# Optimization experiments

Measured on AMD Instinct MI355X. Metric: run time of the kernel, lower is better.

The kernel has to match this reference:

```python
import jax, jax.numpy as jnp
import numpy as np

B = 16384
MOTION = 128      # motion_size
USED = 3          # used_motions
LAT = 32          # latent_size
H1 = 512
H2 = 512
MOE = 8
IN = MOTION * (USED - 1) + LAT  # 288 (used_angles = 0)


def setup_inputs() -> dict:
    key = jax.random.key(0)
    ks = jax.random.split(key, 14)
    s = 0.02
    return {
        "motions": jax.random.normal(ks[0], (B, MOTION * (USED - 1)), jnp.float32),
        "z": jax.random.normal(ks[1], (B, LAT), jnp.float32),
        # gate MLP params
        "gw1": jax.random.normal(ks[2], (IN, H1), jnp.float32) * s,
        "gb1": jnp.zeros((H1,), jnp.float32),
        "gw2": jax.random.normal(ks[3], (H1, H2), jnp.float32) * s,
        "gb2": jnp.zeros((H2,), jnp.float32),
        "gw3": jax.random.normal(ks[4], (H2, MOE), jnp.float32) * s,
        "gb3": jnp.zeros((MOE,), jnp.float32),
        # stacked expert params: layer k weight [MOE, in_k, out_k]
        "W1": jax.random.normal(ks[5], (MOE, IN, H1), jnp.float32) * s,
        "b1": jnp.zeros((MOE, H1), jnp.float32),
        "W2": jax.random.normal(ks[6], (MOE, H1 + LAT, H2), jnp.float32) * s,
        "b2": jnp.zeros((MOE, H2), jnp.float32),
        "W3": jax.random.normal(ks[7], (MOE, H2 + LAT, MOTION), jnp.float32) * s,
        "b3": jnp.zeros((MOE, MOTION), jnp.float32),
    }


def reference(motions, z, gw1, gb1, gw2, gb2, gw3, gb3, W1, b1, W2, b2, W3, b3):
    # used_angles == 0 -> angles is empty; input = concat([motions, z])
    x = jnp.concatenate([motions, z], axis=1)            # [B, IN]

    # gate: 3-layer ELU MLP -> per-expert blend weights [B, MOE]
    para = jax.nn.elu(x @ gw1 + gb1)
    para = jax.nn.elu(para @ gw2 + gb2)
    para = jax.nn.elu(para @ gw3 + gb3)

    # all experts batched via stacked weights (replaces Python loop)
    zb = jnp.broadcast_to(z[None], (MOE, B, LAT))        # z re-concatenated per layer
    h = jax.nn.elu(jnp.einsum('bi,eio->ebo', x, W1) + b1[:, None, :])              # [E,B,H1]
    h = jax.nn.elu(jnp.einsum('ebi,eio->ebo', jnp.concatenate([h, zb], -1), W2)
                   + b2[:, None, :])                                               # [E,B,H2]
    h = jax.nn.elu(jnp.einsum('ebi,eio->ebo', jnp.concatenate([h, zb], -1), W3)
                   + b3[:, None, :])                                               # [E,B,M]

    # gated combine, then divide by Frobenius norm of the whole gate matrix
    out = jnp.einsum('be,ebm->bm', para, h)              # [B, MOTION]
    out = out / jnp.linalg.norm(para)
    return jax.nn.sigmoid(out)
```

## Files before the change

### kernel.cpp

```cpp
#include <hip/hip_runtime.h>


typedef __attribute__((ext_vector_type(8))) short bf16x8;
typedef __attribute__((ext_vector_type(4))) float f32x4;
#define MFMA(a, b, c) __builtin_amdgcn_mfma_f32_16x16x32_bf16(a, b, c, 0, 0, 0)

#define STRIDE 552
#define XSTRIDE 296

__device__ __forceinline__ float elu_f(float x) { return x > 0.f ? x : (__expf(x) - 1.f); }

__device__ __forceinline__ ushort f2bf(float f) {
    union { float f; unsigned u; } v; v.f = f;
    unsigned r = v.u + 0x7fffu + ((v.u >> 16) & 1u);
    return (ushort)(r >> 16);
}
__device__ __forceinline__ float bf2f(ushort u) {
    union { unsigned u; float f; } v; v.u = ((unsigned)u) << 16;
    return v.f;
}
__device__ __forceinline__ bf16x8 ldg8(const ushort* p) { return *(const bf16x8*)p; }

__global__ void prep_xz(const float* __restrict__ motions, const float* __restrict__ z,
                        ushort* __restrict__ xz) {
    int i = blockIdx.x * 256 + threadIdx.x;
    int r = i / 72, c = i % 72;
    float4 v = (c < 64) ? ((const float4*)motions)[r * 64 + c]
                        : ((const float4*)z)[r * 8 + (c - 64)];
    ushort4 o;
    o.x = f2bf(v.x); o.y = f2bf(v.y); o.z = f2bf(v.z); o.w = f2bf(v.w);
    *(ushort4*)(xz + (size_t)r * 288 + c * 4) = o;
}

__global__ void prep_transpose(const float* __restrict__ in, ushort* __restrict__ out,
                               int K, int N) {
    __shared__ float tile[32][33];
    const int e = blockIdx.z;
    const float* inp = in + (size_t)e * K * N;
    ushort* outp = out + (size_t)e * N * K;
    const int k0 = blockIdx.x * 32, n0 = blockIdx.y * 32;
    const int tx = threadIdx.x, ty = threadIdx.y;
    #pragma unroll
    for (int i = 0; i < 4; ++i)
        tile[ty + i * 8][tx] = inp[(size_t)(k0 + ty + i * 8) * N + n0 + tx];
    __syncthreads();
    #pragma unroll
    for (int i = 0; i < 4; ++i)
        outp[(size_t)(n0 + ty + i * 8) * K + k0 + tx] = f2bf(tile[tx][ty + i * 8]);
}

__global__ __launch_bounds__(1024, 1) void gate_kernel(
    const ushort* __restrict__ xz,
    const ushort* __restrict__ gw1t, const float* __restrict__ gb1,
    const ushort* __restrict__ gw2t, const float* __restrict__ gb2,
    const float* __restrict__ gw3, const float* __restrict__ gb3,
    float* __restrict__ para, float* __restrict__ partial)
{
    __shared__ ushort hs[64 * STRIDE];
    __shared__ float red[512];
    const int t = threadIdx.x;
    const int lane = t & 63, w = t >> 6;
    const int lr = lane & 15, lk = lane >> 4;
    const int r0 = blockIdx.x * 64;
    const ushort* xrow = xz + (size_t)r0 * 288;
    const int n0 = w * 32;

    {
        const ushort* B0 = gw1t + (size_t)(n0 + lr) * 288 + lk * 8;
        const ushort* B1 = gw1t + (size_t)(n0 + 16 + lr) * 288 + lk * 8;
        f32x4 acc[4][2] = {};
        bf16x8 bc0 = ldg8(B0), bc1 = ldg8(B1);
        for (int ks = 0; ks < 9; ++ks) {
            bf16x8 bn0 = bc0, bn1 = bc1;
            if (ks < 8) { bn0 = ldg8(B0 + (ks + 1) * 32); bn1 = ldg8(B1 + (ks + 1) * 32); }
            bf16x8 a[4];
            #pragma unroll
            for (int mf = 0; mf < 4; ++mf)
                a[mf] = ldg8(xrow + (size_t)(mf * 16 + lr) * 288 + ks * 32 + lk * 8);
            #pragma unroll
            for (int mf = 0; mf < 4; ++mf) {
                acc[mf][0] = MFMA(a[mf], bc0, acc[mf][0]);
                acc[mf][1] = MFMA(a[mf], bc1, acc[mf][1]);
            }
            bc0 = bn0; bc1 = bn1;
        }
        #pragma unroll
        for (int nf = 0; nf < 2; ++nf) {
            int col = n0 + nf * 16 + lr;
            float bb = gb1[col];
            #pragma unroll
            for (int mf = 0; mf < 4; ++mf)
                #pragma unroll
                for (int j = 0; j < 4; ++j)
                    hs[(mf * 16 + lk * 4 + j) * STRIDE + col] = f2bf(elu_f(acc[mf][nf][j] + bb));
        }
    }
    __syncthreads();

    {
        const ushort* B0 = gw2t + (size_t)(n0 + lr) * 512 + lk * 8;
        const ushort* B1 = gw2t + (size_t)(n0 + 16 + lr) * 512 + lk * 8;
        f32x4 acc[4][2] = {};
        bf16x8 bc0 = ldg8(B0), bc1 = ldg8(B1);
        for (int ks = 0; ks < 16; ++ks) {
            bf16x8 bn0 = bc0, bn1 = bc1;
            if (ks < 15) { bn0 = ldg8(B0 + (ks + 1) * 32); bn1 = ldg8(B1 + (ks + 1) * 32); }
            bf16x8 a[4];
            #pragma unroll
            for (int mf = 0; mf < 4; ++mf)
                a[mf] = *(const bf16x8*)&hs[(mf * 16 + lr) * STRIDE + ks * 32 + lk * 8];
            #pragma unroll
            for (int mf = 0; mf < 4; ++mf) {
                acc[mf][0] = MFMA(a[mf], bc0, acc[mf][0]);
                acc[mf][1] = MFMA(a[mf], bc1, acc[mf][1]);
            }
            bc0 = bn0; bc1 = bn1;
        }
        __syncthreads();
        #pragma unroll
        for (int nf = 0; nf < 2; ++nf) {
            int col = n0 + nf * 16 + lr;
            float bb = gb2[col];
            #pragma unroll
            for (int mf = 0; mf < 4; ++mf)
                #pragma unroll
                for (int j = 0; j < 4; ++j)
                    hs[(mf * 16 + lk * 4 + j) * STRIDE + col] = f2bf(elu_f(acc[mf][nf][j] + bb));
        }
    }
    __syncthreads();

    if (t < 512) {
        const int row = t >> 3, e = t & 7;
        float acc = 0.f;
        for (int k = 0; k < 512; k += 8) {
            uint4 hv = *(const uint4*)&hs[row * STRIDE + k];
            acc += bf2f((ushort)(hv.x)) * gw3[(k + 0) * 8 + e];
            acc += bf2f((ushort)(hv.x >> 16)) * gw3[(k + 1) * 8 + e];
            acc += bf2f((ushort)(hv.y)) * gw3[(k + 2) * 8 + e];
            acc += bf2f((ushort)(hv.y >> 16)) * gw3[(k + 3) * 8 + e];
            acc += bf2f((ushort)(hv.z)) * gw3[(k + 4) * 8 + e];
            acc += bf2f((ushort)(hv.z >> 16)) * gw3[(k + 5) * 8 + e];
            acc += bf2f((ushort)(hv.w)) * gw3[(k + 6) * 8 + e];
            acc += bf2f((ushort)(hv.w >> 16)) * gw3[(k + 7) * 8 + e];
        }
        float p = elu_f(acc + gb3[e]);
        para[(size_t)(r0 + row) * 8 + e] = p;
        red[t] = p * p;
    }
    __syncthreads();
    for (int s = 256; s >= 1; s >>= 1) {
        if (t < s) red[t] += red[t + s];
        __syncthreads();
    }
    if (t == 0) partial[blockIdx.x] = red[0];
}

__global__ void finalize_kernel(const float* __restrict__ partial, float* __restrict__ invn) {
    __shared__ float red[256];
    const int t = threadIdx.x;
    red[t] = partial[t];
    __syncthreads();
    for (int s = 128; s >= 1; s >>= 1) {
        if (t < s) red[t] += red[t + s];
        __syncthreads();
    }
    if (t == 0) invn[0] = 1.0f / sqrtf(red[0]);
}

__global__ __launch_bounds__(1024, 1) void expert_kernel(
    const ushort* __restrict__ xz, const float* __restrict__ z,
    const ushort* __restrict__ W1t, const float* __restrict__ b1,
    const ushort* __restrict__ W2t, const float* __restrict__ b2,
    const ushort* __restrict__ W3t, const float* __restrict__ b3,
    const float* __restrict__ para, const float* __restrict__ invn,
    float* __restrict__ out)
{
    __shared__ ushort hs[64 * STRIDE];
    __shared__ ushort xs[64 * XSTRIDE];
    __shared__ float ps[64 * 8];
    const int t = threadIdx.x;
    const int lane = t & 63, w = t >> 6;
    const int lr = lane & 15, lk = lane >> 4;
    const int r0 = blockIdx.x * 64;
    const int n0 = w * 32;
    const int rb = (w >> 2) * 16;
    const int c0 = (w & 3) * 32;

    for (int i = t; i < 2304; i += 1024) {
        int r = i / 36, c = i % 36;
        *(uint4*)&xs[r * XSTRIDE + c * 8] = *(const uint4*)(xz + (size_t)(r0 + r) * 288 + c * 8);
    }
    for (int i = t; i < 2048; i += 1024) {
        int r = i >> 5, c = i & 31;
        hs[r * STRIDE + 512 + c] = f2bf(z[(size_t)(r0 + r) * 32 + c]);
    }
    if (t < 512) ps[t] = para[(size_t)r0 * 8 + t];
    const float inv_norm = invn[0];

    f32x4 oacc[2] = {};

    for (int e = 0; e < 8; ++e) {
        __syncthreads();

        {
            const ushort* Wt = W1t + (size_t)e * 512 * 288;
            const ushort* B0 = Wt + (size_t)(n0 + lr) * 288 + lk * 8;
            const ushort* B1 = Wt + (size_t)(n0 + 16 + lr) * 288 + lk * 8;
            f32x4 acc[4][2] = {};
            bf16x8 bc0 = ldg8(B0), bc1 = ldg8(B1);
            for (int ks = 0; ks < 9; ++ks) {
                bf16x8 bn0 = bc0, bn1 = bc1;
                if (ks < 8) { bn0 = ldg8(B0 + (ks + 1) * 32); bn1 = ldg8(B1 + (ks + 1) * 32); }
                bf16x8 a[4];
                #pragma unroll
                for (int mf = 0; mf < 4; ++mf)
                    a[mf] = *(const bf16x8*)&xs[(mf * 16 + lr) * XSTRIDE + ks * 32 + lk * 8];
                #pragma unroll
                for (int mf = 0; mf < 4; ++mf) {
                    acc[mf][0] = MFMA(a[mf], bc0, acc[mf][0]);
                    acc[mf][1] = MFMA(a[mf], bc1, acc[mf][1]);
                }
                bc0 = bn0; bc1 = bn1;
            }
            #pragma unroll
            for (int nf = 0; nf < 2; ++nf) {
                int col = n0 + nf * 16 + lr;
                float bb = b1[e * 512 + col];
                #pragma unroll
                for (int mf = 0; mf < 4; ++mf)
                    #pragma unroll
                    for (int j = 0; j < 4; ++j)
                        hs[(mf * 16 + lk * 4 + j) * STRIDE + col] = f2bf(elu_f(acc[mf][nf][j] + bb));
            }
        }
        __syncthreads();

        {
            const ushort* Wt = W2t + (size_t)e * 512 * 544;
            const ushort* B0 = Wt + (size_t)(n0 + lr) * 544 + lk * 8;
            const ushort* B1 = Wt + (size_t)(n0 + 16 + lr) * 544 + lk * 8;
            f32x4 acc[4][2] = {};
            bf16x8 bc0 = ldg8(B0), bc1 = ldg8(B1);
            for (int ks = 0; ks < 17; ++ks) {
                bf16x8 bn0 = bc0, bn1 = bc1;
                if (ks < 16) { bn0 = ldg8(B0 + (ks + 1) * 32); bn1 = ldg8(B1 + (ks + 1) * 32); }
                bf16x8 a[4];
                #pragma unroll
                for (int mf = 0; mf < 4; ++mf)
                    a[mf] = *(const bf16x8*)&hs[(mf * 16 + lr) * STRIDE + ks * 32 + lk * 8];
                #pragma unroll
                for (int mf = 0; mf < 4; ++mf) {
                    acc[mf][0] = MFMA(a[mf], bc0, acc[mf][0]);
                    acc[mf][1] = MFMA(a[mf], bc1, acc[mf][1]);
                }
                bc0 = bn0; bc1 = bn1;
            }
            __syncthreads();
            #pragma unroll
            for (int nf = 0; nf < 2; ++nf) {
                int col = n0 + nf * 16 + lr;
                float bb = b2[e * 512 + col];
                #pragma unroll
                for (int mf = 0; mf < 4; ++mf)
                    #pragma unroll
                    for (int j = 0; j < 4; ++j)
                        hs[(mf * 16 + lk * 4 + j) * STRIDE + col] = f2bf(elu_f(acc[mf][nf][j] + bb));
            }
        }
        __syncthreads();

        {
            const ushort* Wt = W3t + (size_t)e * 128 * 544;
            const ushort* B0 = Wt + (size_t)(c0 + lr) * 544 + lk * 8;
            const ushort* B1 = Wt + (size_t)(c0 + 16 + lr) * 544 + lk * 8;
            f32x4 acc3[2] = {};
            bf16x8 bc0 = ldg8(B0), bc1 = ldg8(B1);
            for (int ks = 0; ks < 17; ++ks) {
                bf16x8 bn0 = bc0, bn1 = bc1;
                if (ks < 16) { bn0 = ldg8(B0 + (ks + 1) * 32); bn1 = ldg8(B1 + (ks + 1) * 32); }
                bf16x8 a = *(const bf16x8*)&hs[(rb + lr) * STRIDE + ks * 32 + lk * 8];
                acc3[0] = MFMA(a, bc0, acc3[0]);
                acc3[1] = MFMA(a, bc1, acc3[1]);
                bc0 = bn0; bc1 = bn1;
            }
            #pragma unroll
            for (int nf = 0; nf < 2; ++nf) {
                float bb = b3[e * 128 + c0 + nf * 16 + lr];
                #pragma unroll
                for (int j = 0; j < 4; ++j) {
                    int row = rb + lk * 4 + j;
                    float h3 = elu_f(acc3[nf][j] + bb);
                    oacc[nf][j] += ps[row * 8 + e] * h3;
                }
            }
        }
    }

    #pragma unroll
    for (int nf = 0; nf < 2; ++nf)
        #pragma unroll
        for (int j = 0; j < 4; ++j) {
            int row = rb + lk * 4 + j;
            float v = oacc[nf][j] * inv_norm;
            out[(size_t)(r0 + row) * 128 + c0 + nf * 16 + lr] = 1.0f / (1.0f + __expf(-v));
        }
}

extern "C" void kernel_launch(void* const* d_in, const int* in_sizes, int n_in,
                              void* d_out, int out_size, void* d_ws, size_t ws_size,
                              hipStream_t stream) {
    const float* motions = (const float*)d_in[0];
    const float* z   = (const float*)d_in[1];
    const float* gw1 = (const float*)d_in[2];
    const float* gb1 = (const float*)d_in[3];
    const float* gw2 = (const float*)d_in[4];
    const float* gb2 = (const float*)d_in[5];
    const float* gw3 = (const float*)d_in[6];
    const float* gb3 = (const float*)d_in[7];
    const float* W1  = (const float*)d_in[8];
    const float* b1  = (const float*)d_in[9];
    const float* W2  = (const float*)d_in[10];
    const float* b2  = (const float*)d_in[11];
    const float* W3  = (const float*)d_in[12];
    const float* b3  = (const float*)d_in[13];
    float* out = (float*)d_out;

    char* W = (char*)d_ws;
    ushort* xz      = (ushort*)(W);
    ushort* gw1t    = (ushort*)(W + 9437184);
    ushort* gw2t    = (ushort*)(W + 9732096);
    ushort* W1t     = (ushort*)(W + 10256384);
    ushort* W2t     = (ushort*)(W + 12615680);
    ushort* W3t     = (ushort*)(W + 17072128);
    float*  para    = (float*) (W + 18186240);
    float*  partial = (float*) (W + 18710528);
    float*  invn    = (float*) (W + 18711552);

    prep_xz<<<dim3(4608), dim3(256), 0, stream>>>(motions, z, xz);
    prep_transpose<<<dim3(9, 16, 1), dim3(32, 8), 0, stream>>>(gw1, gw1t, 288, 512);
    prep_transpose<<<dim3(16, 16, 1), dim3(32, 8), 0, stream>>>(gw2, gw2t, 512, 512);
    prep_transpose<<<dim3(9, 16, 8), dim3(32, 8), 0, stream>>>(W1, W1t, 288, 512);
    prep_transpose<<<dim3(17, 16, 8), dim3(32, 8), 0, stream>>>(W2, W2t, 544, 512);
    prep_transpose<<<dim3(17, 4, 8), dim3(32, 8), 0, stream>>>(W3, W3t, 544, 128);

    gate_kernel<<<dim3(256), dim3(1024), 0, stream>>>(xz, gw1t, gb1, gw2t, gb2, gw3, gb3,
                                                      para, partial);
    finalize_kernel<<<dim3(1), dim3(256), 0, stream>>>(partial, invn);
    expert_kernel<<<dim3(256), dim3(1024), 0, stream>>>(xz, z, W1t, b1, W2t, b2, W3t, b3,
                                                        para, invn, out);
}
```

Baseline: 283.7 us.

## Split experts across two block halves and combine partials in a separate kernel

The expert kernel now launches 512 blocks, with each half handling four experts for a 64-row tile, and writes unnormalized partial sums to two buffers. A new combine kernel adds the partials, applies the inverse norm and the sigmoid. The shared-memory staging of the input tile is removed in favour of direct global loads, and launch bounds ask for two blocks per CU so occupancy can rise on a 256-CU part. The cost is an extra output-sized round trip through memory, an extra launch, and heavier register pressure under the tighter bounds.

```diff
diff --git a/kernel.cpp b/kernel.cpp
--- a/kernel.cpp
+++ b/kernel.cpp
@@ -6,7 +6,6 @@
 #define MFMA(a, b, c) __builtin_amdgcn_mfma_f32_16x16x32_bf16(a, b, c, 0, 0, 0)
 
 #define STRIDE 552
-#define XSTRIDE 296
 
 __device__ __forceinline__ float elu_f(float x) { return x > 0.f ? x : (__expf(x) - 1.f); }
 
@@ -168,39 +167,37 @@
     if (t == 0) invn[0] = 1.0f / sqrtf(red[0]);
 }
 
-__global__ __launch_bounds__(1024, 1) void expert_kernel(
+__global__ __launch_bounds__(1024, 2) void expert_kernel(
     const ushort* __restrict__ xz, const float* __restrict__ z,
     const ushort* __restrict__ W1t, const float* __restrict__ b1,
     const ushort* __restrict__ W2t, const float* __restrict__ b2,
     const ushort* __restrict__ W3t, const float* __restrict__ b3,
-    const float* __restrict__ para, const float* __restrict__ invn,
-    float* __restrict__ out)
+    const float* __restrict__ para,
+    float* __restrict__ part0, float* __restrict__ part1)
 {
     __shared__ ushort hs[64 * STRIDE];
-    __shared__ ushort xs[64 * XSTRIDE];
     __shared__ float ps[64 * 8];
     const int t = threadIdx.x;
     const int lane = t & 63, w = t >> 6;
     const int lr = lane & 15, lk = lane >> 4;
-    const int r0 = blockIdx.x * 64;
+    const int tile = blockIdx.x & 255;
+    const int half = blockIdx.x >> 8;
+    const int r0 = tile * 64;
+    const ushort* xrow = xz + (size_t)r0 * 288;
     const int n0 = w * 32;
     const int rb = (w >> 2) * 16;
     const int c0 = (w & 3) * 32;
 
-    for (int i = t; i < 2304; i += 1024) {
-        int r = i / 36, c = i % 36;
-        *(uint4*)&xs[r * XSTRIDE + c * 8] = *(const uint4*)(xz + (size_t)(r0 + r) * 288 + c * 8);
-    }
     for (int i = t; i < 2048; i += 1024) {
         int r = i >> 5, c = i & 31;
         hs[r * STRIDE + 512 + c] = f2bf(z[(size_t)(r0 + r) * 32 + c]);
     }
     if (t < 512) ps[t] = para[(size_t)r0 * 8 + t];
-    const float inv_norm = invn[0];
 
     f32x4 oacc[2] = {};
-
-    for (int e = 0; e < 8; ++e) {
+    const int e0 = half * 4;
+
+    for (int e = e0; e < e0 + 4; ++e) {
         __syncthreads();
 
         {
@@ -215,7 +212,7 @@
                 bf16x8 a[4];
                 #pragma unroll
                 for (int mf = 0; mf < 4; ++mf)
-                    a[mf] = *(const bf16x8*)&xs[(mf * 16 + lr) * XSTRIDE + ks * 32 + lk * 8];
+                    a[mf] = ldg8(xrow + (size_t)(mf * 16 + lr) * 288 + ks * 32 + lk * 8);
                 #pragma unroll
                 for (int mf = 0; mf < 4; ++mf) {
                     acc[mf][0] = MFMA(a[mf], bc0, acc[mf][0]);
@@ -297,14 +294,27 @@
         }
     }
 
+    float* dst = half ? part1 : part0;
     #pragma unroll
     for (int nf = 0; nf < 2; ++nf)
         #pragma unroll
         for (int j = 0; j < 4; ++j) {
             int row = rb + lk * 4 + j;
-            float v = oacc[nf][j] * inv_norm;
-            out[(size_t)(r0 + row) * 128 + c0 + nf * 16 + lr] = 1.0f / (1.0f + __expf(-v));
-        }
+            dst[(size_t)(r0 + row) * 128 + c0 + nf * 16 + lr] = oacc[nf][j];
+        }
+}
+
+__global__ void combine_kernel(float* __restrict__ out, const float* __restrict__ part1,
+                               const float* __restrict__ invn) {
+    const int i = blockIdx.x * 256 + threadIdx.x;
+    const float inv = invn[0];
+    float4 a = ((const float4*)out)[i];
+    float4 b = ((const float4*)part1)[i];
+    a.x = 1.0f / (1.0f + __expf(-(a.x + b.x) * inv));
+    a.y = 1.0f / (1.0f + __expf(-(a.y + b.y) * inv));
+    a.z = 1.0f / (1.0f + __expf(-(a.z + b.z) * inv));
+    a.w = 1.0f / (1.0f + __expf(-(a.w + b.w) * inv));
+    ((float4*)out)[i] = a;
 }
 
 extern "C" void kernel_launch(void* const* d_in, const int* in_sizes, int n_in,
@@ -336,6 +346,7 @@
     float*  para    = (float*) (W + 18186240);
     float*  partial = (float*) (W + 18710528);
     float*  invn    = (float*) (W + 18711552);
+    float*  part1   = (float*) (W + 18720768);
 
     prep_xz<<<dim3(4608), dim3(256), 0, stream>>>(motions, z, xz);
     prep_transpose<<<dim3(9, 16, 1), dim3(32, 8), 0, stream>>>(gw1, gw1t, 288, 512);
@@ -347,6 +358,7 @@
     gate_kernel<<<dim3(256), dim3(1024), 0, stream>>>(xz, gw1t, gb1, gw2t, gb2, gw3, gb3,
                                                       para, partial);
     finalize_kernel<<<dim3(1), dim3(256), 0, stream>>>(partial, invn);
-    expert_kernel<<<dim3(256), dim3(1024), 0, stream>>>(xz, z, W1t, b1, W2t, b2, W3t, b3,
-                                                        para, invn, out);
-}
+    expert_kernel<<<dim3(512), dim3(1024), 0, stream>>>(xz, z, W1t, b1, W2t, b2, W3t, b3,
+                                                        para, out, part1);
+    combine_kernel<<<dim3(2048), dim3(256), 0, stream>>>(out, part1, invn);
+}
```

Result: slower. 462.8 us (+63.1%).
